# Kernel tuning notes

Hardware: AMD Instinct MI355X
Metric: run time of the kernel (lower is better)

## Reference

```python
import jax, jax.numpy as jnp
import numpy as np

N = 100000   # nodes
E = 1600000  # edges (avg degree 16)
IN = 128     # in_channels
H = 256      # hidden_channels
L = 3        # num_layers
C = 2        # num_classes
EPS = 1e-5   # BatchNorm eps


def setup_inputs() -> dict:
    key = jax.random.key(0)
    ks = jax.random.split(key, 8)
    s = 0.05
    x = jax.random.normal(ks[0], (N, IN), jnp.float32)
    edge_index = jax.random.randint(ks[1], (2, E), 0, N)
    return dict(
        x=x,
        edge_index=edge_index,
        proj_w=jax.random.normal(ks[2], (IN, H), jnp.float32) * s,
        proj_b=jnp.zeros((H,), jnp.float32),
        lin_l_w=jax.random.normal(ks[3], (L, H, H), jnp.float32) * s,
        lin_l_b=jnp.zeros((L, H), jnp.float32),
        lin_r_w=jax.random.normal(ks[4], (L, H, H), jnp.float32) * s,
        bn_g=jnp.ones((L, H), jnp.float32),
        bn_b=jnp.zeros((L, H), jnp.float32),
        fc1_w=jax.random.normal(ks[5], (H, H // 2), jnp.float32) * s,
        fc1_b=jnp.zeros((H // 2,), jnp.float32),
        fc2_w=jax.random.normal(ks[6], (H // 2, C), jnp.float32) * s,
        fc2_b=jnp.zeros((C,), jnp.float32),
    )


def reference(x, edge_index, proj_w, proj_b, lin_l_w, lin_l_b, lin_r_w,
              bn_g, bn_b, fc1_w, fc1_b, fc2_w, fc2_b):
    src, dst = edge_index[0], edge_index[1]
    # in-degree for mean aggregation (SAGEConv aggr='mean')
    deg = jax.ops.segment_sum(jnp.ones((E,), x.dtype), dst, num_segments=N)
    inv_deg = (1.0 / jnp.maximum(deg, 1.0))[:, None]  # [N,1]

    h = jax.nn.relu(x @ proj_w + proj_b)  # [N,H]; dropout is identity in eval
    for i in range(L):
        # SAGEConv: lin_l(mean_{j in N(i)} h_j) + lin_r(h_i)
        agg = jax.ops.segment_sum(h[src], dst, num_segments=N) * inv_deg  # [N,H]
        out = agg @ lin_l_w[i] + lin_l_b[i] + h @ lin_r_w[i]
        # BatchNorm over nodes (batch statistics, biased variance)
        mu = out.mean(axis=0)
        var = out.var(axis=0)
        out = (out - mu) * jax.lax.rsqrt(var + EPS) * bn_g[i] + bn_b[i]
        out = jax.nn.relu(out)
        h = out + h if i > 0 else out  # residual from layer 1 onward

    embeddings = h
    z = jax.nn.relu(embeddings @ fc1_w + fc1_b)
    logits = z @ fc2_w + fc2_b
    return (logits, embeddings)
```

## Files before the change

### kernel.cpp

```cpp
#include <hip/hip_runtime.h>
#include <stdint.h>

#define NN 100000
#define NE 1600000
#define INC 128
#define HID 256
#define MP  100096
#define NBK 391
#define EPB 2048

typedef unsigned short u16;
typedef __attribute__((ext_vector_type(2))) float f32x2;
typedef __attribute__((ext_vector_type(4))) float f32x4;
typedef __attribute__((ext_vector_type(8))) short s16x8;

static __device__ __forceinline__ float bf2f(u16 u){
  union { uint32_t i; float f; } v; v.i = ((uint32_t)u) << 16; return v.f;
}
static __device__ __forceinline__ u16 f2bf(float f){
  union { float f; uint32_t i; } v; v.f = f;
  uint32_t r = v.i + 0x7FFFu + ((v.i >> 16) & 1u);
  return (u16)(r >> 16);
}
static __device__ __forceinline__ void up8(uint4 o, float* v){
  v[0]=bf2f((u16)(o.x&0xffffu)); v[1]=bf2f((u16)(o.x>>16));
  v[2]=bf2f((u16)(o.y&0xffffu)); v[3]=bf2f((u16)(o.y>>16));
  v[4]=bf2f((u16)(o.z&0xffffu)); v[5]=bf2f((u16)(o.z>>16));
  v[6]=bf2f((u16)(o.w&0xffffu)); v[7]=bf2f((u16)(o.w>>16));
}
static __device__ __forceinline__ uint4 pk8(const float* v){
  uint4 o;
  o.x = (uint32_t)f2bf(v[0]) | ((uint32_t)f2bf(v[1])<<16);
  o.y = (uint32_t)f2bf(v[2]) | ((uint32_t)f2bf(v[3])<<16);
  o.z = (uint32_t)f2bf(v[4]) | ((uint32_t)f2bf(v[5])<<16);
  o.w = (uint32_t)f2bf(v[6]) | ((uint32_t)f2bf(v[7])<<16);
  return o;
}
static __device__ __forceinline__ uint2 pkf8(const float* r){
  uint32_t lo = __builtin_amdgcn_cvt_pk_fp8_f32(r[0], r[1], 0u, false);
  lo = __builtin_amdgcn_cvt_pk_fp8_f32(r[2], r[3], lo, true);
  uint32_t hi = __builtin_amdgcn_cvt_pk_fp8_f32(r[4], r[5], 0u, false);
  hi = __builtin_amdgcn_cvt_pk_fp8_f32(r[6], r[7], hi, true);
  return make_uint2(lo, hi);
}

static __device__ __forceinline__ void gload16(const void* g, void* l){
  __builtin_amdgcn_global_load_lds((const __attribute__((address_space(1))) void*)g,
                                   (__attribute__((address_space(3))) void*)l, 16, 0, 0);
}

static __device__ __forceinline__ void packw(const float* __restrict__ src, u16* __restrict__ dst,
                                             int K, int NC, int ksoff, int t){
  int k = t / NC, n = t % NC;
  int NT = NC >> 4;
  int ks = ksoff + (k >> 5);
  int l  = ((k >> 3) & 3)*16 + (n & 15);
  int j  = k & 7;
  dst[((size_t)(ks*NT + (n>>4))*64 + l)*8 + j] = f2bf(src[(size_t)k*NC + n]);
}


__global__ __launch_bounds__(256) void prep_k(
    const float* __restrict__ x, u16* __restrict__ xbf,
    const float* __restrict__ proj_w, u16* __restrict__ wp_proj,
    const float* __restrict__ lin_l_w, const float* __restrict__ lin_r_w,
    u16* __restrict__ wp_l0, u16* __restrict__ wp_l1, u16* __restrict__ wp_l2,
    const float* __restrict__ fc1_w, u16* __restrict__ wp_fc1,
    float* __restrict__ bnacc, int* __restrict__ bcnt)
{
  int b = blockIdx.x;
  int tid = threadIdx.x;
  if (b < 12500){
    int i = b*256 + tid;
    float4 v = ((const float4*)x)[i];
    uint2 o;
    o.x = (uint32_t)f2bf(v.x) | ((uint32_t)f2bf(v.y)<<16);
    o.y = (uint32_t)f2bf(v.z) | ((uint32_t)f2bf(v.w)<<16);
    ((uint2*)xbf)[i] = o;
    return;
  }
  b -= 12500;
  if (b < 128){ packw(proj_w, wp_proj, 128, 256, 0, b*256 + tid); return; }
  b -= 128;
  if (b < 1536){
    int wsel = b >> 8;
    int t = (b & 255)*256 + tid;
    int i = wsel >> 1;
    u16* dst = (i == 0) ? wp_l0 : (i == 1) ? wp_l1 : wp_l2;
    if (wsel & 1) packw(lin_r_w + (size_t)i*65536, dst, 256, 256, 8, t);
    else          packw(lin_l_w + (size_t)i*65536, dst, 256, 256, 0, t);
    return;
  }
  b -= 1536;
  if (b < 128){ packw(fc1_w, wp_fc1, 256, 128, 0, b*256 + tid); return; }
  b -= 128;
  {
    int i = b*256 + tid;
    if (i < 3*8192) bnacc[i] = 0.f;
    if (i < NBK) bcnt[i] = 0;
  }
}


__global__ __launch_bounds__(256) void bhist_k(const int* __restrict__ ei, int* __restrict__ bcnt){
  __shared__ int h[NBK];
  for (int i = threadIdx.x; i < NBK; i += 256) h[i] = 0;
  __syncthreads();
  int e0 = blockIdx.x * EPB;
  #pragma unroll
  for (int j = 0; j < EPB/256; ++j){
    int e = e0 + j*256 + threadIdx.x;
    if (e < NE) atomicAdd(&h[ei[NE + e] >> 8], 1);
  }
  __syncthreads();
  for (int i = threadIdx.x; i < NBK; i += 256)
    if (h[i]) atomicAdd(&bcnt[i], h[i]);
}

__global__ __launch_bounds__(512) void bscan_k(const int* __restrict__ bcnt, int* __restrict__ bcur){
  __shared__ int sd[512];
  int t = threadIdx.x;
  int v = (t < NBK) ? bcnt[t] : 0;
  sd[t] = v; __syncthreads();
  for (int o = 1; o < 512; o <<= 1){
    int x = (t >= o) ? sd[t-o] : 0;
    __syncthreads();
    sd[t] += x;
    __syncthreads();
  }
  if (t < NBK) bcur[t] = sd[t] - v;
}

__global__ __launch_bounds__(256) void bfill_k(const int* __restrict__ ei, int* __restrict__ bcur,
                                               unsigned* __restrict__ epair){
  __shared__ int cnt[NBK];
  __shared__ int gb[NBK];
  for (int i = threadIdx.x; i < NBK; i += 256) cnt[i] = 0;
  __syncthreads();
  int e0 = blockIdx.x * EPB;
  unsigned pk[EPB/256];
  int bkt[EPB/256], rnk[EPB/256];
  #pragma unroll
  for (int j = 0; j < EPB/256; ++j){
    int e = e0 + j*256 + threadIdx.x;
    if (e < NE){
      int s = ei[e];
      int d = ei[NE + e];
      bkt[j] = d >> 8;
      pk[j]  = ((unsigned)s << 8) | (unsigned)(d & 255);
      rnk[j] = atomicAdd(&cnt[bkt[j]], 1);
    } else bkt[j] = -1;
  }
  __syncthreads();
  for (int i = threadIdx.x; i < NBK; i += 256){
    int c = cnt[i];
    gb[i] = c ? atomicAdd(&bcur[i], c) : 0;
  }
  __syncthreads();
  #pragma unroll
  for (int j = 0; j < EPB/256; ++j){
    if (bkt[j] >= 0)
      epair[gb[bkt[j]] + rnk[j]] = pk[j];
  }
}

__global__ __launch_bounds__(256) void csort_k(const unsigned* __restrict__ epair,
                                               const int* __restrict__ bcnt, const int* __restrict__ bcur,
                                               int* __restrict__ ci, int* __restrict__ rp){
  __shared__ int hist[256], pfx[256], cnt2[256];
  int b = blockIdx.x, t = threadIdx.x;
  int cnt  = bcnt[b];
  int base = bcur[b] - cnt;
  hist[t] = 0; cnt2[t] = 0;
  __syncthreads();
  for (int e = t; e < cnt; e += 256)
    atomicAdd(&hist[epair[base + e] & 255u], 1);
  __syncthreads();
  int v = hist[t];
  pfx[t] = v;
  __syncthreads();
  for (int o = 1; o < 256; o <<= 1){
    int x = (t >= o) ? pfx[t - o] : 0;
    __syncthreads();
    pfx[t] += x;
    __syncthreads();
  }
  int node = b*256 + t;
  if (node < NN) rp[node] = base + pfx[t] - v;
  if (b == NBK-1 && t == 0) rp[NN] = NE;
  for (int e = t; e < cnt; e += 256){
    unsigned p = epair[base + e];
    int ld = (int)(p & 255u);
    int r  = atomicAdd(&cnt2[ld], 1);
    ci[base + pfx[ld] - hist[ld] + r] = (int)(p >> 8);
  }
}


__global__ __launch_bounds__(256) void agg8_k(const int* __restrict__ rp, const int* __restrict__ ci,
                                              const uint4* __restrict__ h8, u16* __restrict__ ag){
  int wid  = (int)((blockIdx.x*256u + threadIdx.x) >> 6);
  int lane = threadIdx.x & 63;
  int ql   = lane & 15;
  int w    = wid*4 + (lane >> 4);
  bool act = (w < NN);
  int e0 = 0, e1 = 0;
  if (act){ e0 = rp[w]; e1 = rp[w+1]; }
  int cnt = e1 - e0;

  float a[16];
  #pragma unroll
  for (int k = 0; k < 16; ++k) a[k] = 0.f;

  for (int base = 0; __any(base < cnt); base += 16){
    int rem = cnt - base;
    int my = 0;
    if (ql < rem) my = ci[e0 + base + ql];
    #pragma unroll
    for (int j0 = 0; j0 < 16; j0 += 8){
      if (!__any(j0 < rem)) break;
      uint4 v[8];
      #pragma unroll
      for (int jj = 0; jj < 8; ++jj){
        int j = j0 + jj;
        int s = __shfl(my, (lane & 48) + j);
        v[jj] = make_uint4(0,0,0,0);
        if (j < rem) v[jj] = h8[(size_t)s*16 + ql];
      }
      #pragma unroll
      for (int jj = 0; jj < 8; ++jj){
        uint32_t wd[4] = {v[jj].x, v[jj].y, v[jj].z, v[jj].w};
        #pragma unroll
        for (int p = 0; p < 4; ++p){
          f32x2 lo = __builtin_amdgcn_cvt_pk_f32_fp8(wd[p], false);
          f32x2 hi = __builtin_amdgcn_cvt_pk_f32_fp8(wd[p], true);
          a[p*4+0] += lo[0]; a[p*4+1] += lo[1];
          a[p*4+2] += hi[0]; a[p*4+3] += hi[1];
        }
      }
    }
  }

  if (act){
    float inv = 1.0f / (float)(cnt > 0 ? cnt : 1);
    float r0[8], r1[8];
    #pragma unroll
    for (int k = 0; k < 8; ++k){ r0[k] = a[k]*inv; r1[k] = a[8+k]*inv; }
    uint4* agu = (uint4*)ag;
    agu[(size_t)w*32 + ql*2]     = pk8(r0);
    agu[(size_t)w*32 + ql*2 + 1] = pk8(r1);
  }
}


__global__ __launch_bounds__(256) void aggb_k(const int* __restrict__ rp, const int* __restrict__ ci,
                                              const u16* __restrict__ h, u16* __restrict__ ag){
  int w = (int)((blockIdx.x*256u + threadIdx.x) >> 6);
  int lane = threadIdx.x & 63;
  if (w >= NN) return;
  int e0 = rp[w], e1 = rp[w+1];
  const uint2* hu = (const uint2*)h;
  float a0=0.f, a1=0.f, a2=0.f, a3=0.f;
  for (int base = e0; base < e1; base += 64){
    int cnt = e1 - base; if (cnt > 64) cnt = 64;
    int my = ci[base + (lane < cnt ? lane : cnt-1)];
    int i = 0;
    for (; i + 8 <= cnt; i += 8){
      int s[8];
      #pragma unroll
      for (int jj = 0; jj < 8; ++jj) s[jj] = __builtin_amdgcn_readlane(my, i + jj);
      uint2 v[8];
      #pragma unroll
      for (int jj = 0; jj < 8; ++jj) v[jj] = hu[(size_t)s[jj]*64 + lane];
      #pragma unroll
      for (int jj = 0; jj < 8; ++jj){
        a0 += bf2f((u16)(v[jj].x & 0xffffu));
        a1 += bf2f((u16)(v[jj].x >> 16));
        a2 += bf2f((u16)(v[jj].y & 0xffffu));
        a3 += bf2f((u16)(v[jj].y >> 16));
      }
    }
    for (; i < cnt; ++i){
      int s0 = __builtin_amdgcn_readlane(my, i);
      uint2 v = hu[(size_t)s0*64 + lane];
      a0 += bf2f((u16)(v.x&0xffffu));
      a1 += bf2f((u16)(v.x>>16));
      a2 += bf2f((u16)(v.y&0xffffu));
      a3 += bf2f((u16)(v.y>>16));
    }
  }
  int d = e1 - e0;
  float inv = 1.0f / (float)(d > 0 ? d : 1);
  uint2 o;
  o.x = (uint32_t)f2bf(a0*inv) | ((uint32_t)f2bf(a1*inv) << 16);
  o.y = (uint32_t)f2bf(a2*inv) | ((uint32_t)f2bf(a3*inv) << 16);
  ((uint2*)ag)[(size_t)w*64 + lane] = o;
}


template<int KS1, int KS2, int NCC, int EPI>
__global__ __launch_bounds__(256, 3) void gemm3_k(
    const u16* __restrict__ A1, const u16* __restrict__ A2,
    const u16* __restrict__ Wp, const float* __restrict__ bias,
    u16* __restrict__ Cout, int M, float* __restrict__ stS,
    const float* __restrict__ w2, const float* __restrict__ b2, float* __restrict__ out2)
{
  constexpr int NT    = NCC >> 4;
  constexpr int NFRAG = NCC / 64;
  constexpr int NS1   = KS1 / 2;
  constexpr int NSTEP = (KS1 + KS2) / 2;

  __shared__ u16 Al[2][64*64];
  __shared__ float red[4][64][2];

  const int t    = threadIdx.x;
  const int lane = t & 63;
  const int wv   = t >> 6;
  const int r15  = lane & 15, kg = lane >> 4;
  const int rb   = blockIdx.x * 64;
  const int nt0w = wv * NFRAG;

  f32x4 acc[4][NFRAG];
  #pragma unroll
  for (int m = 0; m < 4; ++m)
    #pragma unroll
    for (int n = 0; n < NFRAG; ++n){ f32x4 z = {0.f,0.f,0.f,0.f}; acc[m][n] = z; }

  auto stageA = [&](int step, int bsel){
    const bool inA1 = (step < NS1);
    const u16* Ab   = inA1 ? A1 : A2;
    const int  Krow = (inA1 ? KS1 : KS2) * 32;
    const int  kloc = (inA1 ? step : step - NS1) * 64;
    #pragma unroll
    for (int c = 0; c < 2; ++c){
      int row = c*32 + wv*8 + (lane >> 3);
      int gc  = (lane & 7) ^ (row & 7);
      const u16* g = Ab + (size_t)(rb + row)*Krow + kloc + gc*8;
      gload16(g, &Al[bsel][c*2048 + wv*512]);
    }
  };
  auto loadB = [&](int ss, s16x8* dst){
    const u16* g = Wp + ((size_t)(ss*NT + nt0w)*64 + lane)*8;
    #pragma unroll
    for (int n = 0; n < NFRAG; ++n)
      dst[n] = *(const s16x8*)(g + (size_t)n*512);
  };

  s16x8 bb[2][NFRAG];
  stageA(0, 0);
  loadB(0, bb[0]);
  __syncthreads();

  #pragma unroll
  for (int step = 0; step < NSTEP; ++step){
    const int cur = step & 1;
    if (step + 1 < NSTEP) stageA(step + 1, cur ^ 1);
    #pragma unroll
    for (int sl = 0; sl < 2; ++sl){
      const int ss = step*2 + sl;
      const int p  = ss & 1;
      if (ss + 1 < NSTEP*2) loadB(ss + 1, bb[p ^ 1]);
      s16x8 af[4];
      const char* Ab = (const char*)&Al[cur][0];
      #pragma unroll
      for (int m = 0; m < 4; ++m){
        int row = m*16 + r15;
        int c16 = (sl*4 + kg) ^ (row & 7);
        af[m] = *(const s16x8*)(Ab + row*128 + c16*16);
      }
      #pragma unroll
      for (int m = 0; m < 4; ++m)
        #pragma unroll
        for (int n = 0; n < NFRAG; ++n)
          acc[m][n] = __builtin_amdgcn_mfma_f32_16x16x32_bf16(af[m], bb[p][n], acc[m][n], 0, 0, 0);
    }
    __syncthreads();
  }

  if (EPI == 2){
    float p[4][4][2];
    #pragma unroll
    for (int m = 0; m < 4; ++m)
      #pragma unroll
      for (int r = 0; r < 4; ++r){ p[m][r][0] = 0.f; p[m][r][1] = 0.f; }
    #pragma unroll
    for (int n = 0; n < NFRAG; ++n){
      int col = (nt0w + n)*16 + r15;
      float bc = bias[col];
      float w0 = w2[col*2], w1 = w2[col*2 + 1];
      #pragma unroll
      for (int m = 0; m < 4; ++m)
        #pragma unroll
        for (int r = 0; r < 4; ++r){
          float val = fmaxf(acc[m][n][r] + bc, 0.f);
          p[m][r][0] += val*w0;
          p[m][r][1] += val*w1;
        }
    }
    #pragma unroll
    for (int off = 1; off < 16; off <<= 1)
      #pragma unroll
      for (int m = 0; m < 4; ++m)
        #pragma unroll
        for (int r = 0; r < 4; ++r){
          p[m][r][0] += __shfl_xor(p[m][r][0], off);
          p[m][r][1] += __shfl_xor(p[m][r][1], off);
        }
    if (r15 == 0){
      #pragma unroll
      for (int m = 0; m < 4; ++m)
        #pragma unroll
        for (int r = 0; r < 4; ++r){
          red[wv][m*16 + kg*4 + r][0] = p[m][r][0];
          red[wv][m*16 + kg*4 + r][1] = p[m][r][1];
        }
    }
    __syncthreads();
    if (t < 128){
      int row = t >> 1, c = t & 1;
      float s = red[0][row][c] + red[1][row][c] + red[2][row][c] + red[3][row][c] + b2[c];
      if (rb + row < M) out2[(size_t)(rb + row)*2 + c] = s;
    }
    return;
  }

  #pragma unroll
  for (int n = 0; n < NFRAG; ++n){
    int col = (nt0w + n)*16 + r15;
    float bc = bias[col];
    float s = 0.f, q = 0.f;
    #pragma unroll
    for (int m = 0; m < 4; ++m){
      int rbase = rb + m*16 + kg*4;
      #pragma unroll
      for (int r = 0; r < 4; ++r){
        int row = rbase + r;
        float val = acc[m][n][r] + bc;
        if (EPI == 0) val = fmaxf(val, 0.f);
        bool ok = row < M;
        if (ok) Cout[(size_t)row*NCC + col] = f2bf(val);
        if (EPI == 1 && ok){ s += val; q += val*val; }
      }
    }
    if (EPI == 1){
      s += __shfl_xor(s, 16); s += __shfl_xor(s, 32);
      q += __shfl_xor(q, 16); q += __shfl_xor(q, 32);
      if (lane < 16){
        int idx = ((blockIdx.x & 15) << 9) + col;
        atomicAdd(&stS[idx], s);
        atomicAdd(&stS[idx + 256], q);
      }
    }
  }
}


__global__ __launch_bounds__(256) void bnfin_k(const float* __restrict__ acc,
                                               const float* __restrict__ g, const float* __restrict__ b,
                                               float* __restrict__ coef){
  int c = threadIdx.x;
  float s = 0.f, q = 0.f;
  #pragma unroll
  for (int j = 0; j < 16; ++j){
    s += acc[j*512 + c];
    q += acc[j*512 + 256 + c];
  }
  float mean = s * (1.0f / (float)NN);
  float var  = q * (1.0f / (float)NN) - mean*mean;
  float sc = g[c] * rsqrtf(var + 1e-5f);
  coef[c] = sc;
  coef[256 + c] = b[c] - mean*sc;
}

__global__ __launch_bounds__(256) void bnapply_k(const uint4* __restrict__ outb, uint4* __restrict__ h,
                                                 uint2* __restrict__ h8,
                                                 const float* __restrict__ coef, int layer, int wr8,
                                                 float* __restrict__ embout){
  int i = blockIdx.x*256 + threadIdx.x;
  if (i >= NN*32) return;
  int col0 = (i & 31) * 8;
  const float4* scp = (const float4*)(coef + col0);
  const float4* shp = (const float4*)(coef + 256 + col0);
  float4 s0 = scp[0], s1 = scp[1], t0 = shp[0], t1 = shp[1];
  float sc[8] = {s0.x,s0.y,s0.z,s0.w,s1.x,s1.y,s1.z,s1.w};
  float sh[8] = {t0.x,t0.y,t0.z,t0.w,t1.x,t1.y,t1.z,t1.w};
  float v[8], r[8];
  up8(outb[i], v);
  #pragma unroll
  for (int j = 0; j < 8; ++j) r[j] = fmaxf(v[j]*sc[j] + sh[j], 0.f);
  if (layer > 0){
    float hv[8];
    up8(h[i], hv);
    #pragma unroll
    for (int j = 0; j < 8; ++j) r[j] += hv[j];
  }
  h[i] = pk8(r);
  if (wr8) h8[i] = pkf8(r);
  if (embout){
    int row = i >> 5;
    float4* ep = (float4*)(embout + (size_t)row*256 + col0);
    ep[0] = make_float4(r[0], r[1], r[2], r[3]);
    ep[1] = make_float4(r[4], r[5], r[6], r[7]);
  }
}

__global__ __launch_bounds__(256) void cvt8_k(const uint4* __restrict__ h, uint2* __restrict__ h8, int n){
  int i = blockIdx.x*256 + threadIdx.x;
  if (i >= n) return;
  float v[8];
  up8(h[i], v);
  h8[i] = pkf8(v);
}


extern "C" void kernel_launch(void* const* d_in, const int* in_sizes, int n_in,
                              void* d_out, int out_size, void* d_ws, size_t ws_size,
                              hipStream_t stream){
  const float* x       = (const float*)d_in[0];
  const int*   ei      = (const int*)d_in[1];
  const float* proj_w  = (const float*)d_in[2];
  const float* proj_b  = (const float*)d_in[3];
  const float* lin_l_w = (const float*)d_in[4];
  const float* lin_l_b = (const float*)d_in[5];
  const float* lin_r_w = (const float*)d_in[6];
  const float* bn_g    = (const float*)d_in[7];
  const float* bn_b    = (const float*)d_in[8];
  const float* fc1_w   = (const float*)d_in[9];
  const float* fc1_b   = (const float*)d_in[10];
  const float* fc2_w   = (const float*)d_in[11];
  const float* fc2_b   = (const float*)d_in[12];
  float* out = (float*)d_out;

  char* ws = (char*)d_ws;
  size_t off = 0;
  auto alloc = [&](size_t b){ size_t o = off; off = (off + b + 255) & ~(size_t)255; return o; };

  u16* bufA    = (u16*)(ws + alloc((size_t)MP*256*2));
  u16* hbuf    = (u16*)(ws + alloc((size_t)MP*256*2));
  u16* bufC    = (u16*)(ws + alloc((size_t)MP*256*2));
  uint8_t* h8  = (uint8_t*)(ws + alloc((size_t)MP*256));
  u16* wp_proj = (u16*)(ws + alloc((size_t)4*16*64*8*2));
  u16* wp_l[3];
  for (int i = 0; i < 3; ++i) wp_l[i] = (u16*)(ws + alloc((size_t)16*16*64*8*2));
  u16* wp_fc1  = (u16*)(ws + alloc((size_t)8*8*64*8*2));
  int* rp    = (int*)(ws + alloc((size_t)(NN+1)*4));
  int* ci    = (int*)(ws + alloc((size_t)NE*4));
  int* bcnt  = (int*)(ws + alloc(NBK*4));
  int* bcur  = (int*)(ws + alloc(NBK*4));
  float* bnacc = (float*)(ws + alloc(3*8192*4));
  float* coef  = (float*)(ws + alloc(3*512*4));
  unsigned* epair = (unsigned*)bufC;
  (void)ws_size; (void)in_sizes; (void)n_in; (void)out_size;

  const int BFB = (NE + EPB - 1)/EPB;
  const int GX = MP/64;
  const int PREPB = 12500 + 128 + 1536 + 128 + 96;

  prep_k<<<PREPB, 256, 0, stream>>>(x, bufA, proj_w, wp_proj, lin_l_w, lin_r_w,
                                    wp_l[0], wp_l[1], wp_l[2], fc1_w, wp_fc1, bnacc, bcnt);

  bhist_k<<<BFB, 256, 0, stream>>>(ei, bcnt);
  bscan_k<<<1, 512, 0, stream>>>(bcnt, bcur);
  bfill_k<<<BFB, 256, 0, stream>>>(ei, bcur, epair);
  csort_k<<<NBK, 256, 0, stream>>>(epair, bcnt, bcur, ci, rp);

  gemm3_k<4,0,256,0><<<GX, 256, 0, stream>>>(bufA, nullptr, wp_proj, proj_b,
                                             hbuf, NN, nullptr, nullptr, nullptr, nullptr);
  cvt8_k<<<(NN*32 + 255)/256, 256, 0, stream>>>((const uint4*)hbuf, (uint2*)h8, NN*32);

  for (int i = 0; i < 3; ++i){
    if (i < 2)
      agg8_k<<<((NN + 3)/4*64 + 255)/256, 256, 0, stream>>>(rp, ci, (const uint4*)h8, bufA);
    else
      aggb_k<<<(NN + 3)/4, 256, 0, stream>>>(rp, ci, hbuf, bufA);
    gemm3_k<8,8,256,1><<<GX, 256, 0, stream>>>(bufA, hbuf, wp_l[i], lin_l_b + (size_t)i*256,
                                               bufC, NN, bnacc + i*8192, nullptr, nullptr, nullptr);
    bnfin_k<<<1, 256, 0, stream>>>(bnacc + i*8192, bn_g + (size_t)i*256, bn_b + (size_t)i*256, coef + i*512);
    bnapply_k<<<(NN*32 + 255)/256, 256, 0, stream>>>((const uint4*)bufC, (uint4*)hbuf, (uint2*)h8,
                                                     coef + i*512, i, (i == 0) ? 1 : 0,
                                                     (i == 2) ? (out + 200000) : nullptr);
  }

  gemm3_k<8,0,128,2><<<GX, 256, 0, stream>>>(hbuf, nullptr, wp_fc1, fc1_b,
                                             nullptr, NN, nullptr, fc2_w, fc2_b, out);
}
```

Before: 646.4 us.

## Fuse neighbor mean aggregation into the SAGE layer GEMM via shared memory

Result: slower. 706.2 us (+9.2%).

```diff
diff --git a/kernel.cpp b/kernel.cpp
--- a/kernel.cpp
+++ b/kernel.cpp
@@ -197,118 +197,222 @@
 }
 
 
-__global__ __launch_bounds__(256) void agg8_k(const int* __restrict__ rp, const int* __restrict__ ci,
-                                              const uint4* __restrict__ h8, u16* __restrict__ ag){
-  int wid  = (int)((blockIdx.x*256u + threadIdx.x) >> 6);
-  int lane = threadIdx.x & 63;
-  int ql   = lane & 15;
-  int w    = wid*4 + (lane >> 4);
-  bool act = (w < NN);
-  int e0 = 0, e1 = 0;
-  if (act){ e0 = rp[w]; e1 = rp[w+1]; }
-  int cnt = e1 - e0;
-
-  float a[16];
-  #pragma unroll
-  for (int k = 0; k < 16; ++k) a[k] = 0.f;
-
-  for (int base = 0; __any(base < cnt); base += 16){
-    int rem = cnt - base;
-    int my = 0;
-    if (ql < rem) my = ci[e0 + base + ql];
-    #pragma unroll
-    for (int j0 = 0; j0 < 16; j0 += 8){
-      if (!__any(j0 < rem)) break;
-      uint4 v[8];
-      #pragma unroll
-      for (int jj = 0; jj < 8; ++jj){
-        int j = j0 + jj;
-        int s = __shfl(my, (lane & 48) + j);
-        v[jj] = make_uint4(0,0,0,0);
-        if (j < rem) v[jj] = h8[(size_t)s*16 + ql];
+template<int FP8>
+__global__ __launch_bounds__(256, 3) void fgemm_k(
+    const int* __restrict__ rp, const int* __restrict__ ci,
+    const void* __restrict__ hsrc,
+    const u16* __restrict__ A2,
+    const u16* __restrict__ Wp, const float* __restrict__ bias,
+    u16* __restrict__ Cout, int M, float* __restrict__ stS)
+{
+  __shared__ u16 aggL[64*256];
+  __shared__ u16 Al[2][64*64];
+
+  const int t    = threadIdx.x;
+  const int lane = t & 63;
+  const int wv   = t >> 6;
+  const int r15  = lane & 15, kg = lane >> 4;
+  const int rb   = blockIdx.x * 64;
+  const int nt0w = wv * 4;
+
+  auto stageA = [&](int step, int bsel){
+    #pragma unroll
+    for (int c = 0; c < 2; ++c){
+      int row = c*32 + wv*8 + (lane >> 3);
+      int gc  = (lane & 7) ^ (row & 7);
+      const u16* g = A2 + (size_t)(rb + row)*256 + step*64 + gc*8;
+      gload16(g, &Al[bsel][c*2048 + wv*512]);
+    }
+  };
+  stageA(0, 0);
+
+  if (FP8){
+    const uint4* h8 = (const uint4*)hsrc;
+    int ql = lane & 15;
+    #pragma unroll 1
+    for (int it = 0; it < 4; ++it){
+      int r = wv*16 + it*4 + (lane >> 4);
+      int w = rb + r;
+      int e0 = 0, e1 = 0;
+      if (w < NN){ e0 = rp[w]; e1 = rp[w+1]; }
+      int cnt = e1 - e0;
+      float a[16];
+      #pragma unroll
+      for (int k = 0; k < 16; ++k) a[k] = 0.f;
+      for (int base = 0; __any(base < cnt); base += 16){
+        int rem = cnt - base;
+        int my = 0;
+        if (ql < rem) my = ci[e0 + base + ql];
+        #pragma unroll
+        for (int j0 = 0; j0 < 16; j0 += 8){
+          if (!__any(j0 < rem)) break;
+          uint4 v[8];
+          #pragma unroll
+          for (int jj = 0; jj < 8; ++jj){
+            int j = j0 + jj;
+            int s = __shfl(my, (lane & 48) + j);
+            v[jj] = make_uint4(0,0,0,0);
+            if (j < rem) v[jj] = h8[(size_t)s*16 + ql];
+          }
+          #pragma unroll
+          for (int jj = 0; jj < 8; ++jj){
+            uint32_t wd[4] = {v[jj].x, v[jj].y, v[jj].z, v[jj].w};
+            #pragma unroll
+            for (int p = 0; p < 4; ++p){
+              f32x2 lo = __builtin_amdgcn_cvt_pk_f32_fp8(wd[p], false);
+              f32x2 hi = __builtin_amdgcn_cvt_pk_f32_fp8(wd[p], true);
+              a[p*4+0] += lo[0]; a[p*4+1] += lo[1];
+              a[p*4+2] += hi[0]; a[p*4+3] += hi[1];
+            }
+          }
+        }
       }
-      #pragma unroll
-      for (int jj = 0; jj < 8; ++jj){
-        uint32_t wd[4] = {v[jj].x, v[jj].y, v[jj].z, v[jj].w};
-        #pragma unroll
-        for (int p = 0; p < 4; ++p){
-          f32x2 lo = __builtin_amdgcn_cvt_pk_f32_fp8(wd[p], false);
-          f32x2 hi = __builtin_amdgcn_cvt_pk_f32_fp8(wd[p], true);
-          a[p*4+0] += lo[0]; a[p*4+1] += lo[1];
-          a[p*4+2] += hi[0]; a[p*4+3] += hi[1];
+      float inv = 1.0f / (float)(cnt > 0 ? cnt : 1);
+      float r0[8], r1[8];
+      #pragma unroll
+      for (int k = 0; k < 8; ++k){ r0[k] = a[k]*inv; r1[k] = a[8+k]*inv; }
+      char* rowb = (char*)aggL + r*512;
+      *(uint4*)(rowb + ((ql*2    ) ^ (r & 7))*16) = pk8(r0);
+      *(uint4*)(rowb + ((ql*2 + 1) ^ (r & 7))*16) = pk8(r1);
+    }
+  } else {
+    const uint2* hu = (const uint2*)hsrc;
+    #pragma unroll 1
+    for (int it = 0; it < 16; ++it){
+      int r = wv*16 + it;
+      int w = rb + r;
+      int e0 = 0, e1 = 0;
+      if (w < NN){ e0 = rp[w]; e1 = rp[w+1]; }
+      float a0=0.f, a1=0.f, a2=0.f, a3=0.f;
+      for (int base = e0; base < e1; base += 64){
+        int cnt = e1 - base; if (cnt > 64) cnt = 64;
+        int my = ci[base + (lane < cnt ? lane : cnt-1)];
+        int i = 0;
+        for (; i + 8 <= cnt; i += 8){
+          int s[8];
+          #pragma unroll
+          for (int jj = 0; jj < 8; ++jj) s[jj] = __builtin_amdgcn_readlane(my, i + jj);
+          uint2 v[8];
+          #pragma unroll
+          for (int jj = 0; jj < 8; ++jj) v[jj] = hu[(size_t)s[jj]*64 + lane];
+          #pragma unroll
+          for (int jj = 0; jj < 8; ++jj){
+            a0 += bf2f((u16)(v[jj].x & 0xffffu));
+            a1 += bf2f((u16)(v[jj].x >> 16));
+            a2 += bf2f((u16)(v[jj].y & 0xffffu));
+            a3 += bf2f((u16)(v[jj].y >> 16));
+          }
+        }
+        for (; i < cnt; ++i){
+          int s0 = __builtin_amdgcn_readlane(my, i);
+          uint2 v = hu[(size_t)s0*64 + lane];
+          a0 += bf2f((u16)(v.x&0xffffu));
+          a1 += bf2f((u16)(v.x>>16));
+          a2 += bf2f((u16)(v.y&0xffffu));
+          a3 += bf2f((u16)(v.y>>16));
         }
       }
-    }
-  }
-
-  if (act){
-    float inv = 1.0f / (float)(cnt > 0 ? cnt : 1);
-    float r0[8], r1[8];
-    #pragma unroll
-    for (int k = 0; k < 8; ++k){ r0[k] = a[k]*inv; r1[k] = a[8+k]*inv; }
-    uint4* agu = (uint4*)ag;
-    agu[(size_t)w*32 + ql*2]     = pk8(r0);
-    agu[(size_t)w*32 + ql*2 + 1] = pk8(r1);
-  }
-}
-
-
-__global__ __launch_bounds__(256) void aggb_k(const int* __restrict__ rp, const int* __restrict__ ci,
-                                              const u16* __restrict__ h, u16* __restrict__ ag){
-  int w = (int)((blockIdx.x*256u + threadIdx.x) >> 6);
-  int lane = threadIdx.x & 63;
-  if (w >= NN) return;
-  int e0 = rp[w], e1 = rp[w+1];
-  const uint2* hu = (const uint2*)h;
-  float a0=0.f, a1=0.f, a2=0.f, a3=0.f;
-  for (int base = e0; base < e1; base += 64){
-    int cnt = e1 - base; if (cnt > 64) cnt = 64;
-    int my = ci[base + (lane < cnt ? lane : cnt-1)];
-    int i = 0;
-    for (; i + 8 <= cnt; i += 8){
-      int s[8];
-      #pragma unroll
-      for (int jj = 0; jj < 8; ++jj) s[jj] = __builtin_amdgcn_readlane(my, i + jj);
-      uint2 v[8];
-      #pragma unroll
-      for (int jj = 0; jj < 8; ++jj) v[jj] = hu[(size_t)s[jj]*64 + lane];
-      #pragma unroll
-      for (int jj = 0; jj < 8; ++jj){
-        a0 += bf2f((u16)(v[jj].x & 0xffffu));
-        a1 += bf2f((u16)(v[jj].x >> 16));
-        a2 += bf2f((u16)(v[jj].y & 0xffffu));
-        a3 += bf2f((u16)(v[jj].y >> 16));
+      int d = e1 - e0;
+      float inv = 1.0f / (float)(d > 0 ? d : 1);
+      uint2 o;
+      o.x = (uint32_t)f2bf(a0*inv) | ((uint32_t)f2bf(a1*inv) << 16);
+      o.y = (uint32_t)f2bf(a2*inv) | ((uint32_t)f2bf(a3*inv) << 16);
+      *(uint2*)((char*)aggL + r*512 + (((lane >> 1) ^ (r & 7))*16) + (lane & 1)*8) = o;
+    }
+  }
+  __syncthreads();
+
+  f32x4 acc[4][4];
+  #pragma unroll
+  for (int m = 0; m < 4; ++m)
+    #pragma unroll
+    for (int n = 0; n < 4; ++n){ f32x4 z = {0.f,0.f,0.f,0.f}; acc[m][n] = z; }
+
+  auto loadB = [&](int ss, s16x8* dst){
+    const u16* g = Wp + ((size_t)(ss*16 + nt0w)*64 + lane)*8;
+    #pragma unroll
+    for (int n = 0; n < 4; ++n)
+      dst[n] = *(const s16x8*)(g + (size_t)n*512);
+  };
+
+  s16x8 bb[2][4];
+  loadB(0, bb[0]);
+
+  #pragma unroll
+  for (int st = 0; st < 8; ++st){
+    if (st == 0) stageA(1, 1);
+    if (st == 5) stageA(2, 0);
+    if (st == 6) stageA(3, 1);
+    #pragma unroll
+    for (int sl = 0; sl < 2; ++sl){
+      const int ss = st*2 + sl;
+      if (ss + 1 < 16) loadB(ss + 1, bb[(ss + 1) & 1]);
+      s16x8 af[4];
+      if (st < 4){
+        #pragma unroll
+        for (int m = 0; m < 4; ++m){
+          int row = m*16 + r15;
+          int kb  = (sl*4 + kg) ^ (row & 7);
+          af[m] = *(const s16x8*)((char*)aggL + row*512 + st*128 + kb*16);
+        }
+      } else {
+        const char* Ab = (const char*)&Al[st & 1][0];
+        #pragma unroll
+        for (int m = 0; m < 4; ++m){
+          int row = m*16 + r15;
+          int c16 = (sl*4 + kg) ^ (row & 7);
+          af[m] = *(const s16x8*)(Ab + row*128 + c16*16);
+        }
       }
-    }
-    for (; i < cnt; ++i){
-      int s0 = __builtin_amdgcn_readlane(my, i);
-      uint2 v = hu[(size_t)s0*64 + lane];
-      a0 += bf2f((u16)(v.x&0xffffu));
-      a1 += bf2f((u16)(v.x>>16));
-      a2 += bf2f((u16)(v.y&0xffffu));
-      a3 += bf2f((u16)(v.y>>16));
-    }
-  }
-  int d = e1 - e0;
-  float inv = 1.0f / (float)(d > 0 ? d : 1);
-  uint2 o;
-  o.x = (uint32_t)f2bf(a0*inv) | ((uint32_t)f2bf(a1*inv) << 16);
-  o.y = (uint32_t)f2bf(a2*inv) | ((uint32_t)f2bf(a3*inv) << 16);
-  ((uint2*)ag)[(size_t)w*64 + lane] = o;
-}
-
-
-template<int KS1, int KS2, int NCC, int EPI>
+      #pragma unroll
+      for (int m = 0; m < 4; ++m)
+        #pragma unroll
+        for (int n = 0; n < 4; ++n)
+          acc[m][n] = __builtin_amdgcn_mfma_f32_16x16x32_bf16(af[m], bb[ss & 1][n], acc[m][n], 0, 0, 0);
+    }
+    if (st >= 4) __syncthreads();
+  }
+
+  #pragma unroll
+  for (int n = 0; n < 4; ++n){
+    int col = (nt0w + n)*16 + r15;
+    float bc = bias[col];
+    float s = 0.f, q = 0.f;
+    #pragma unroll
+    for (int m = 0; m < 4; ++m){
+      int rbase = rb + m*16 + kg*4;
+      #pragma unroll
+      for (int r = 0; r < 4; ++r){
+        int row = rbase + r;
+        float val = acc[m][n][r] + bc;
+        bool ok = row < M;
+        if (ok){
+          Cout[(size_t)row*256 + col] = f2bf(val);
+          s += val; q += val*val;
+        }
+      }
+    }
+    s += __shfl_xor(s, 16); s += __shfl_xor(s, 32);
+    q += __shfl_xor(q, 16); q += __shfl_xor(q, 32);
+    if (lane < 16){
+      int idx = ((blockIdx.x & 15) << 9) + col;
+      atomicAdd(&stS[idx], s);
+      atomicAdd(&stS[idx + 256], q);
+    }
+  }
+}
+
+
+template<int KS1, int NCC, int EPI>
 __global__ __launch_bounds__(256, 3) void gemm3_k(
-    const u16* __restrict__ A1, const u16* __restrict__ A2,
+    const u16* __restrict__ A1,
     const u16* __restrict__ Wp, const float* __restrict__ bias,
-    u16* __restrict__ Cout, int M, float* __restrict__ stS,
+    u16* __restrict__ Cout, int M,
     const float* __restrict__ w2, const float* __restrict__ b2, float* __restrict__ out2)
 {
   constexpr int NT    = NCC >> 4;
   constexpr int NFRAG = NCC / 64;
-  constexpr int NS1   = KS1 / 2;
-  constexpr int NSTEP = (KS1 + KS2) / 2;
+  constexpr int NSTEP = KS1 / 2;
 
   __shared__ u16 Al[2][64*64];
   __shared__ float red[4][64][2];
@@ -327,15 +431,11 @@
     for (int n = 0; n < NFRAG; ++n){ f32x4 z = {0.f,0.f,0.f,0.f}; acc[m][n] = z; }
 
   auto stageA = [&](int step, int bsel){
-    const bool inA1 = (step < NS1);
-    const u16* Ab   = inA1 ? A1 : A2;
-    const int  Krow = (inA1 ? KS1 : KS2) * 32;
-    const int  kloc = (inA1 ? step : step - NS1) * 64;
     #pragma unroll
     for (int c = 0; c < 2; ++c){
       int row = c*32 + wv*8 + (lane >> 3);
       int gc  = (lane & 7) ^ (row & 7);
-      const u16* g = Ab + (size_t)(rb + row)*Krow + kloc + gc*8;
+      const u16* g = A1 + (size_t)(rb + row)*(KS1*32) + step*64 + gc*8;
       gload16(g, &Al[bsel][c*2048 + wv*512]);
     }
   };
@@ -428,27 +528,14 @@
   for (int n = 0; n < NFRAG; ++n){
     int col = (nt0w + n)*16 + r15;
     float bc = bias[col];
-    float s = 0.f, q = 0.f;
     #pragma unroll
     for (int m = 0; m < 4; ++m){
       int rbase = rb + m*16 + kg*4;
       #pragma unroll
       for (int r = 0; r < 4; ++r){
         int row = rbase + r;
-        float val = acc[m][n][r] + bc;
-        if (EPI == 0) val = fmaxf(val, 0.f);
-        bool ok = row < M;
-        if (ok) Cout[(size_t)row*NCC + col] = f2bf(val);
-        if (EPI == 1 && ok){ s += val; q += val*val; }
-      }
-    }
-    if (EPI == 1){
-      s += __shfl_xor(s, 16); s += __shfl_xor(s, 32);
-      q += __shfl_xor(q, 16); q += __shfl_xor(q, 32);
-      if (lane < 16){
-        int idx = ((blockIdx.x & 15) << 9) + col;
-        atomicAdd(&stS[idx], s);
-        atomicAdd(&stS[idx + 256], q);
+        float val = fmaxf(acc[m][n][r] + bc, 0.f);
+        if (row < M) Cout[(size_t)row*NCC + col] = f2bf(val);
       }
     }
   }
@@ -564,23 +651,23 @@
   bfill_k<<<BFB, 256, 0, stream>>>(ei, bcur, epair);
   csort_k<<<NBK, 256, 0, stream>>>(epair, bcnt, bcur, ci, rp);
 
-  gemm3_k<4,0,256,0><<<GX, 256, 0, stream>>>(bufA, nullptr, wp_proj, proj_b,
-                                             hbuf, NN, nullptr, nullptr, nullptr, nullptr);
+  gemm3_k<4,256,0><<<GX, 256, 0, stream>>>(bufA, wp_proj, proj_b,
+                                           hbuf, NN, nullptr, nullptr, nullptr);
   cvt8_k<<<(NN*32 + 255)/256, 256, 0, stream>>>((const uint4*)hbuf, (uint2*)h8, NN*32);
 
   for (int i = 0; i < 3; ++i){
     if (i < 2)
-      agg8_k<<<((NN + 3)/4*64 + 255)/256, 256, 0, stream>>>(rp, ci, (const uint4*)h8, bufA);
+      fgemm_k<1><<<GX, 256, 0, stream>>>(rp, ci, h8, hbuf, wp_l[i], lin_l_b + (size_t)i*256,
+                                         bufC, NN, bnacc + i*8192);
     else
-      aggb_k<<<(NN + 3)/4, 256, 0, stream>>>(rp, ci, hbuf, bufA);
-    gemm3_k<8,8,256,1><<<GX, 256, 0, stream>>>(bufA, hbuf, wp_l[i], lin_l_b + (size_t)i*256,
-                                               bufC, NN, bnacc + i*8192, nullptr, nullptr, nullptr);
+      fgemm_k<0><<<GX, 256, 0, stream>>>(rp, ci, hbuf, hbuf, wp_l[i], lin_l_b + (size_t)i*256,
+                                         bufC, NN, bnacc + i*8192);
     bnfin_k<<<1, 256, 0, stream>>>(bnacc + i*8192, bn_g + (size_t)i*256, bn_b + (size_t)i*256, coef + i*512);
     bnapply_k<<<(NN*32 + 255)/256, 256, 0, stream>>>((const uint4*)bufC, (uint4*)hbuf, (uint2*)h8,
                                                      coef + i*512, i, (i == 0) ? 1 : 0,
                                                      (i == 2) ? (out + 200000) : nullptr);
   }
 
-  gemm3_k<8,0,128,2><<<GX, 256, 0, stream>>>(hbuf, nullptr, wp_fc1, fc1_b,
-                                             nullptr, NN, nullptr, fc2_w, fc2_b, out);
-}
+  gemm3_k<8,128,2><<<GX, 256, 0, stream>>>(hbuf, wp_fc1, fc1_b,
+                                           nullptr, NN, fc2_w, fc2_b, out);
+}
```
